# Optimization experiments

Hardware: AMD Instinct MI355X
Metric: run time of the kernel (lower is better)

The kernel has to match this reference:

```python
import jax, jax.numpy as jnp
import numpy as np

B, T, C = 4, 2048, 768
NH = 12
HD = C // NH  # 64


def setup_inputs() -> dict:
    key = jax.random.key(0)
    k1, k2, k3 = jax.random.split(key, 3)
    x = jax.random.normal(k1, (B, T, C), dtype=jnp.float32)
    W_attn = jax.random.normal(k2, (C, 3 * C), dtype=jnp.float32) * (1.0 / np.sqrt(C))
    b_attn = jnp.zeros((3 * C,), dtype=jnp.float32)
    W_proj = jax.random.normal(k3, (C, C), dtype=jnp.float32) * (1.0 / np.sqrt(C))
    b_proj = jnp.zeros((C,), dtype=jnp.float32)
    return {"x": x, "W_attn": W_attn, "b_attn": b_attn, "W_proj": W_proj, "b_proj": b_proj}


def reference(x, W_attn, b_attn, W_proj, b_proj):
    b, t, c = x.shape
    nh, hd = NH, c // NH
    qkv = x @ W_attn + b_attn                      # (B,T,3C)
    q, k, v = jnp.split(qkv, 3, axis=2)
    # (B,T,C) -> (B,NH,T,HD)
    q = q.reshape(b, t, nh, hd).transpose(0, 2, 1, 3)
    k = k.reshape(b, t, nh, hd).transpose(0, 2, 1, 3)
    v = v.reshape(b, t, nh, hd).transpose(0, 2, 1, 3)
    att = jnp.einsum('bhqd,bhkd->bhqk', q, k) / jnp.sqrt(jnp.float32(hd))
    causal = jnp.tril(jnp.ones((t, t), dtype=bool))
    att = jnp.where(causal, att, -jnp.inf)
    att = jax.nn.softmax(att, axis=-1)
    y = jnp.einsum('bhqk,bhkd->bhqd', att, v)      # (B,NH,T,HD)
    y = y.transpose(0, 2, 1, 3).reshape(b, t, c)
    return y @ W_proj + b_proj
```

## Files before the change

### kernel.cpp

```cpp
#include <hip/hip_runtime.h>
#include <hip/hip_bf16.h>
#include <cstdint>

typedef __bf16 bf16;
typedef __bf16 bf16x4 __attribute__((ext_vector_type(4)));
typedef __bf16 bf16x8 __attribute__((ext_vector_type(8)));
typedef float f32x4 __attribute__((ext_vector_type(4)));

#define B_  4
#define T_  2048
#define C_  768
#define NH_ 12
#define HD_ 64
#define BH_ (B_ * NH_)

__device__ __forceinline__ f32x4 mfma16(bf16x8 a, bf16x8 b, f32x4 c) {
  return __builtin_amdgcn_mfma_f32_16x16x32_bf16(a, b, c, 0, 0, 0);
}

__device__ __forceinline__ void gload16(const bf16* src, bf16* dst) {
  __builtin_amdgcn_global_load_lds(
      (const __attribute__((address_space(1))) unsigned int*)src,
      (__attribute__((address_space(3))) unsigned int*)dst, 16, 0, 0);
}

__global__ __launch_bounds__(256) void cvt_kernel(const float* __restrict__ in,
                                                  bf16* __restrict__ out, int n4) {
  int i = blockIdx.x * blockDim.x + threadIdx.x;
  if (i < n4) {
    float4 v = reinterpret_cast<const float4*>(in)[i];
    bf16x4 o;
    o[0] = (bf16)v.x; o[1] = (bf16)v.y; o[2] = (bf16)v.z; o[3] = (bf16)v.w;
    reinterpret_cast<bf16x4*>(out)[i] = o;
  }
}

__global__ __launch_bounds__(256) void wtr_kernel(const float* __restrict__ W,
                                                  bf16* __restrict__ WT, int K, int N) {
  __shared__ bf16 t[64][72];
  const int tid = threadIdx.x;
  const int k0 = blockIdx.x * 64, n0 = blockIdx.y * 64;
  {
    const int r = tid >> 2, cg = (tid & 3) * 16;
    const float* src = W + (size_t)(k0 + r) * N + n0 + cg;
    float4 a0 = reinterpret_cast<const float4*>(src)[0];
    float4 a1 = reinterpret_cast<const float4*>(src)[1];
    float4 a2 = reinterpret_cast<const float4*>(src)[2];
    float4 a3 = reinterpret_cast<const float4*>(src)[3];
    bf16x8 lo, hi;
    lo[0]=(bf16)a0.x; lo[1]=(bf16)a0.y; lo[2]=(bf16)a0.z; lo[3]=(bf16)a0.w;
    lo[4]=(bf16)a1.x; lo[5]=(bf16)a1.y; lo[6]=(bf16)a1.z; lo[7]=(bf16)a1.w;
    hi[0]=(bf16)a2.x; hi[1]=(bf16)a2.y; hi[2]=(bf16)a2.z; hi[3]=(bf16)a2.w;
    hi[4]=(bf16)a3.x; hi[5]=(bf16)a3.y; hi[6]=(bf16)a3.z; hi[7]=(bf16)a3.w;
    *reinterpret_cast<bf16x8*>(&t[r][cg]) = lo;
    *reinterpret_cast<bf16x8*>(&t[r][cg + 8]) = hi;
  }
  __syncthreads();
  {
    const int n = tid & 63, kg = (tid >> 6) * 16;
    bf16x8 o0, o1;
#pragma unroll
    for (int i = 0; i < 8; ++i) { o0[i] = t[kg + i][n]; o1[i] = t[kg + 8 + i][n]; }
    bf16* dst = WT + (size_t)(n0 + n) * K + k0 + kg;
    *reinterpret_cast<bf16x8*>(dst) = o0;
    *reinterpret_cast<bf16x8*>(dst + 8) = o1;
  }
}

template <int EPI>
__global__ __launch_bounds__(256) void gemm_mfma(
    const bf16* __restrict__ A, const bf16* __restrict__ BT,
    const float* __restrict__ bias, int M, int N, int K,
    bf16* __restrict__ q, bf16* __restrict__ k_, bf16* __restrict__ v,
    float* __restrict__ out) {
  __shared__ bf16 AlF[128 * 64];
  __shared__ bf16 BlF[128 * 64];

  const int tid = threadIdx.x;
  const int wid = tid >> 6, lane = tid & 63;
  unsigned orig = blockIdx.y * gridDim.x + blockIdx.x;
  unsigned cpx = (gridDim.x * gridDim.y) >> 3;
  unsigned work = (orig & 7) * cpx + (orig >> 3);
  const int m0 = (work / gridDim.x) * 128, n0 = (work % gridDim.x) * 128;
  const int wm = (wid >> 1) * 64, wn = (wid & 1) * 64;
  const int r = lane & 15, g = lane >> 4;

  f32x4 acc[4][4] = {};

  const int l8 = lane >> 3;
  const int c8 = (lane & 7) * 8;

  for (int k0 = 0; k0 < K; k0 += 64) {
    __syncthreads();
#pragma unroll
    for (int i = 0; i < 4; ++i) {
      int row = i * 32 + wid * 8 + l8;
      gload16(A  + (size_t)(m0 + row) * K + k0 + c8, AlF + (i * 32 + wid * 8) * 64);
      gload16(BT + (size_t)(n0 + row) * K + k0 + c8, BlF + (i * 32 + wid * 8) * 64);
    }
    __syncthreads();

#pragma unroll
    for (int kc = 0; kc < 2; ++kc) {
      bf16x8 bfr[4];
#pragma unroll
      for (int fn = 0; fn < 4; ++fn)
        bfr[fn] = *reinterpret_cast<bf16x8*>(&BlF[(wn + fn * 16 + r) * 64 + kc * 32 + g * 8]);
#pragma unroll
      for (int fm = 0; fm < 4; ++fm) {
        bf16x8 af = *reinterpret_cast<bf16x8*>(&AlF[(wm + fm * 16 + r) * 64 + kc * 32 + g * 8]);
#pragma unroll
        for (int fn = 0; fn < 4; ++fn)
          acc[fm][fn] = mfma16(af, bfr[fn], acc[fm][fn]);
      }
    }
  }

#pragma unroll
  for (int fm = 0; fm < 4; ++fm)
#pragma unroll
    for (int fn = 0; fn < 4; ++fn)
#pragma unroll
      for (int j = 0; j < 4; ++j) {
        int m = m0 + wm + fm * 16 + g * 4 + j;
        int n = n0 + wn + fn * 16 + r;
        float val = acc[fm][fn][j] + bias[n];
        if (EPI == 0) {
          int b = m >> 11, t = m & 2047;
          bf16* dst; int c;
          if (n < 768)        { dst = q;  c = n;        val *= 0.180336881f; }
          else if (n < 1536)  { dst = k_; c = n - 768;  }
          else                { dst = v;  c = n - 1536; }
          int h = c >> 6, d = c & 63;
          dst[(((size_t)(b * NH_ + h)) * T_ + t) * HD_ + d] = (bf16)val;
        } else {
          out[(size_t)m * N + n] = val;
        }
      }
}

__global__ __launch_bounds__(256) void attn_fwd(
    const bf16* __restrict__ Q, const bf16* __restrict__ K,
    const bf16* __restrict__ V, bf16* __restrict__ Y) {
  __shared__ bf16 Kl[64][72];
  __shared__ bf16 VtF[64 * 72];
  __shared__ bf16 Pl[4][16][72];

  const int tid = threadIdx.x;
  const int wid = tid >> 6, lane = tid & 63;
  const int r = lane & 15, g = lane >> 4;

  unsigned orig = blockIdx.y * 16 + blockIdx.x;
  unsigned work = (orig & 7) * 96 + (orig >> 3);
  const int bx = work & 15;
  const int bh = work >> 4;
  const int bidx = bh / NH_, h = bh % NH_;

  const bf16* Qb = Q + (size_t)bh * T_ * HD_;
  const bf16* Kb = K + (size_t)bh * T_ * HD_;
  const bf16* Vb = V + (size_t)bh * T_ * HD_;

  const int krow = tid >> 3;
  const int kc8 = (tid & 7) * 8;

#pragma unroll
  for (int pass = 0; pass < 2; ++pass) {
    const int tile = pass ? 31 - bx : bx;
    const int qt0 = tile * 64 + wid * 16;

    bf16x8 qf[2];
#pragma unroll
    for (int kc = 0; kc < 2; ++kc)
      qf[kc] = *reinterpret_cast<const bf16x8*>(
          Qb + (size_t)(qt0 + r) * HD_ + kc * 32 + g * 8);

    float m_st = -INFINITY;
    float l_p = 0.f;
    f32x4 o[4] = {};

    const int nsteps = tile + 1;

    bf16x8 kreg[2], vreg[2];
#pragma unroll
    for (int p = 0; p < 2; ++p) {
      int row = p * 32 + krow;
      kreg[p] = *reinterpret_cast<const bf16x8*>(Kb + (size_t)row * HD_ + kc8);
      vreg[p] = *reinterpret_cast<const bf16x8*>(Vb + (size_t)row * HD_ + kc8);
    }

    for (int s = 0; s < nsteps; ++s) {
      const int kv0 = s * 64;
#pragma unroll
      for (int p = 0; p < 2; ++p) {
        int row = p * 32 + krow;
        *reinterpret_cast<bf16x8*>(&Kl[row][kc8]) = kreg[p];
        int xorb = (((row >> 3) ^ (tid & 7)) << 3) + (row & 7);
#pragma unroll
        for (int j = 0; j < 8; ++j) VtF[(kc8 + j) * 72 + xorb] = vreg[p][j];
      }
      __syncthreads();

      if (s + 1 < nsteps) {
        const int kvn = kv0 + 64;
#pragma unroll
        for (int p = 0; p < 2; ++p) {
          int row = kvn + p * 32 + krow;
          kreg[p] = *reinterpret_cast<const bf16x8*>(Kb + (size_t)row * HD_ + kc8);
          vreg[p] = *reinterpret_cast<const bf16x8*>(Vb + (size_t)row * HD_ + kc8);
        }
      }

      f32x4 s4[4] = {};
      __builtin_amdgcn_s_setprio(1);
#pragma unroll
      for (int cb = 0; cb < 4; ++cb)
#pragma unroll
        for (int kc = 0; kc < 2; ++kc) {
          bf16x8 kf = *reinterpret_cast<bf16x8*>(&Kl[cb * 16 + r][kc * 32 + g * 8]);
          s4[cb] = mfma16(kf, qf[kc], s4[cb]);
        }
      __builtin_amdgcn_s_setprio(0);

      if (s == tile) {
#pragma unroll
        for (int cb = 0; cb < 4; ++cb)
#pragma unroll
          for (int j = 0; j < 4; ++j)
            if (kv0 + cb * 16 + g * 4 + j > qt0 + r) s4[cb][j] = -INFINITY;
      }

      float pmax = fmaxf(
          fmaxf(fmaxf(fmaxf(s4[0][0], s4[0][1]), fmaxf(s4[0][2], s4[0][3])),
                fmaxf(fmaxf(s4[1][0], s4[1][1]), fmaxf(s4[1][2], s4[1][3]))),
          fmaxf(fmaxf(fmaxf(s4[2][0], s4[2][1]), fmaxf(s4[2][2], s4[2][3])),
                fmaxf(fmaxf(s4[3][0], s4[3][1]), fmaxf(s4[3][2], s4[3][3]))));
      pmax = fmaxf(pmax, __shfl_xor(pmax, 16));
      pmax = fmaxf(pmax, __shfl_xor(pmax, 32));

      if (!__all(pmax - m_st <= 8.0f)) {
        float sc = exp2f(m_st - pmax);
        m_st = pmax;
        l_p *= sc;
        float sc0 = __shfl(sc, g * 4 + 0);
        float sc1 = __shfl(sc, g * 4 + 1);
        float sc2 = __shfl(sc, g * 4 + 2);
        float sc3 = __shfl(sc, g * 4 + 3);
#pragma unroll
        for (int dn = 0; dn < 4; ++dn) {
          o[dn][0] *= sc0; o[dn][1] *= sc1; o[dn][2] *= sc2; o[dn][3] *= sc3;
        }
      }

      float sum = 0.f;
#pragma unroll
      for (int cb = 0; cb < 4; ++cb) {
        bf16x4 pw;
#pragma unroll
        for (int j = 0; j < 4; ++j) {
          float pv = exp2f(s4[cb][j] - m_st);
          sum += pv;
          pw[j] = (bf16)pv;
        }
        *reinterpret_cast<bf16x4*>(&Pl[wid][r][cb * 16 + g * 4]) = pw;
      }
      l_p += sum;

      __builtin_amdgcn_s_setprio(1);
#pragma unroll
      for (int kc = 0; kc < 2; ++kc) {
        bf16x8 pf = *reinterpret_cast<bf16x8*>(&Pl[wid][r][kc * 32 + g * 8]);
#pragma unroll
        for (int dn = 0; dn < 4; ++dn) {
          int d = dn * 16 + r;
          bf16x8 vf = *reinterpret_cast<bf16x8*>(
              &VtF[d * 72 + (((4 * kc + g) ^ (d >> 3)) << 3)]);
          o[dn] = mfma16(pf, vf, o[dn]);
        }
      }
      __builtin_amdgcn_s_setprio(0);
      __syncthreads();
    }

    l_p += __shfl_xor(l_p, 16);
    l_p += __shfl_xor(l_p, 32);
    float linv = 1.f / l_p;
    float i0 = __shfl(linv, g * 4 + 0);
    float i1 = __shfl(linv, g * 4 + 1);
    float i2 = __shfl(linv, g * 4 + 2);
    float i3 = __shfl(linv, g * 4 + 3);

#pragma unroll
    for (int j = 0; j < 4; ++j) {
      float inv = j == 0 ? i0 : (j == 1 ? i1 : (j == 2 ? i2 : i3));
      int qrow = qt0 + g * 4 + j;
#pragma unroll
      for (int dn = 0; dn < 4; ++dn) {
        int d = dn * 16 + r;
        Y[((size_t)bidx * T_ + qrow) * C_ + h * HD_ + d] = (bf16)(o[dn][j] * inv);
      }
    }
  }
}

extern "C" void kernel_launch(void* const* d_in, const int* in_sizes, int n_in,
                              void* d_out, int out_size, void* d_ws, size_t ws_size,
                              hipStream_t stream) {
  const float* x  = (const float*)d_in[0];
  const float* Wa = (const float*)d_in[1];
  const float* ba = (const float*)d_in[2];
  const float* Wp = (const float*)d_in[3];
  const float* bp = (const float*)d_in[4];
  float* out = (float*)d_out;

  char* ws = (char*)d_ws;
  size_t off = 0;
  auto alloc = [&](size_t bytes) {
    char* p = ws + off;
    off += (bytes + 255) & ~(size_t)255;
    return p;
  };
  bf16* xb   = (bf16*)alloc((size_t)B_ * T_ * C_ * 2);
  bf16* WaT  = (bf16*)alloc((size_t)C_ * 3 * C_ * 2);
  bf16* WpT  = (bf16*)alloc((size_t)C_ * C_ * 2);
  bf16* Qb   = (bf16*)alloc((size_t)BH_ * T_ * HD_ * 2);
  bf16* Kb   = (bf16*)alloc((size_t)BH_ * T_ * HD_ * 2);
  bf16* Vb   = (bf16*)alloc((size_t)BH_ * T_ * HD_ * 2);
  bf16* Yb   = (bf16*)alloc((size_t)B_ * T_ * C_ * 2);

  const int M = B_ * T_;

  cvt_kernel<<<(M * C_ / 4) / 256, 256, 0, stream>>>(x, xb, M * C_ / 4);
  wtr_kernel<<<dim3(C_ / 64, 3 * C_ / 64), 256, 0, stream>>>(Wa, WaT, C_, 3 * C_);
  wtr_kernel<<<dim3(C_ / 64, C_ / 64), 256, 0, stream>>>(Wp, WpT, C_, C_);

  gemm_mfma<0><<<dim3(3 * C_ / 128, M / 128), 256, 0, stream>>>(
      xb, WaT, ba, M, 3 * C_, C_, Qb, Kb, Vb, nullptr);

  attn_fwd<<<dim3(16, BH_), 256, 0, stream>>>(Qb, Kb, Vb, Yb);

  gemm_mfma<1><<<dim3(C_ / 128, M / 128), 256, 0, stream>>>(
      Yb, WpT, bp, M, C_, C_, nullptr, nullptr, nullptr, out);
}
```

Measured before the change: 241.6 us.

## Double-buffer GEMM LDS tiles with BK=32 and prefetch the next tile

```diff
diff --git a/kernel.cpp b/kernel.cpp
--- a/kernel.cpp
+++ b/kernel.cpp
@@ -73,8 +73,8 @@
     const float* __restrict__ bias, int M, int N, int K,
     bf16* __restrict__ q, bf16* __restrict__ k_, bf16* __restrict__ v,
     float* __restrict__ out) {
-  __shared__ bf16 AlF[128 * 64];
-  __shared__ bf16 BlF[128 * 64];
+  __shared__ bf16 AlF[2][128 * 32];
+  __shared__ bf16 BlF[2][128 * 32];
 
   const int tid = threadIdx.x;
   const int wid = tid >> 6, lane = tid & 63;
@@ -87,33 +87,44 @@
 
   f32x4 acc[4][4] = {};
 
-  const int l8 = lane >> 3;
-  const int c8 = (lane & 7) * 8;
-
-  for (int k0 = 0; k0 < K; k0 += 64) {
+  const int srow = tid >> 2;
+  const int scol = (tid & 3) * 8;
+
+#pragma unroll
+  for (int c = 0; c < 2; ++c) {
+    gload16(A  + (size_t)(m0 + c * 64 + srow) * K + scol, &AlF[0][c * 2048 + wid * 512]);
+    gload16(BT + (size_t)(n0 + c * 64 + srow) * K + scol, &BlF[0][c * 2048 + wid * 512]);
+  }
+
+  int cur = 0;
+  for (int k0 = 0; k0 < K; k0 += 32) {
     __syncthreads();
-#pragma unroll
-    for (int i = 0; i < 4; ++i) {
-      int row = i * 32 + wid * 8 + l8;
-      gload16(A  + (size_t)(m0 + row) * K + k0 + c8, AlF + (i * 32 + wid * 8) * 64);
-      gload16(BT + (size_t)(n0 + row) * K + k0 + c8, BlF + (i * 32 + wid * 8) * 64);
+
+    if (k0 + 32 < K) {
+#pragma unroll
+      for (int c = 0; c < 2; ++c) {
+        gload16(A  + (size_t)(m0 + c * 64 + srow) * K + k0 + 32 + scol,
+                &AlF[cur ^ 1][c * 2048 + wid * 512]);
+        gload16(BT + (size_t)(n0 + c * 64 + srow) * K + k0 + 32 + scol,
+                &BlF[cur ^ 1][c * 2048 + wid * 512]);
+      }
     }
-    __syncthreads();
-
-#pragma unroll
-    for (int kc = 0; kc < 2; ++kc) {
-      bf16x8 bfr[4];
+
+    bf16x8 af[4], bfr[4];
+#pragma unroll
+    for (int fm = 0; fm < 4; ++fm)
+      af[fm] = *reinterpret_cast<bf16x8*>(&AlF[cur][(wm + fm * 16 + r) * 32 + g * 8]);
+#pragma unroll
+    for (int fn = 0; fn < 4; ++fn)
+      bfr[fn] = *reinterpret_cast<bf16x8*>(&BlF[cur][(wn + fn * 16 + r) * 32 + g * 8]);
+    __builtin_amdgcn_s_setprio(1);
+#pragma unroll
+    for (int fm = 0; fm < 4; ++fm)
 #pragma unroll
       for (int fn = 0; fn < 4; ++fn)
-        bfr[fn] = *reinterpret_cast<bf16x8*>(&BlF[(wn + fn * 16 + r) * 64 + kc * 32 + g * 8]);
-#pragma unroll
-      for (int fm = 0; fm < 4; ++fm) {
-        bf16x8 af = *reinterpret_cast<bf16x8*>(&AlF[(wm + fm * 16 + r) * 64 + kc * 32 + g * 8]);
-#pragma unroll
-        for (int fn = 0; fn < 4; ++fn)
-          acc[fm][fn] = mfma16(af, bfr[fn], acc[fm][fn]);
-      }
-    }
+        acc[fm][fn] = mfma16(af[fm], bfr[fn], acc[fm][fn]);
+    __builtin_amdgcn_s_setprio(0);
+    cur ^= 1;
   }
 
 #pragma unroll
```

Measured after the change: 237.6 us. Within noise of the previous version (-1.7%).
